# Optimization experiments

Measured on AMD Instinct MI355X. Metric: run time of the kernel, lower is better.

## Reference

```python
import jax, jax.numpy as jnp
import numpy as np

N = 4096      # num utterances (graph nodes)
D = 512       # utt_embed_size * 2
W = 10        # att_window_size
S = 8         # num speakers
WIN = 2 * W + 1


def setup_inputs() -> dict:
    key = jax.random.key(0)
    ks = jax.random.split(key, 7)
    s = 0.05  # keep activations in a sane range through two layers
    return {
        "context_embeds": jax.random.normal(ks[0], (N, D), jnp.float32),
        "speakers": jax.random.randint(ks[1], (N,), 0, S),
        "w_gc1": jax.random.normal(ks[2], (4, D, D), jnp.float32) * s,
        "w_gc2": jax.random.normal(ks[3], (4, D, D), jnp.float32) * s,
        "w_att": jax.random.normal(ks[4], (D, D), jnp.float32) * s,
        "w_aggr1": jax.random.normal(ks[5], (D, D), jnp.float32) * s,
        "w_aggr2": jax.random.normal(ks[6], (D, D), jnp.float32) * s,
    }


def _relation_adjs(x, speakers, w_att):
    """Windowed edge attention + 4 relation-masked adjacency matrices."""
    n = x.shape[0]
    pad = jnp.zeros((W, D), x.dtype)
    padded = jnp.concatenate([pad, x, pad], axis=0)          # [n+2W, D]
    # banded gather: row j sees padded[j : j+2W+1]  == cols j-W .. j+W
    gidx = jnp.arange(n)[:, None] + jnp.arange(WIN)[None, :]
    fat = padded[gidx]
    raw = jnp.einsum('nwd,ed->nwe', fat, w_att)               # Linear: x @ W^T
    scores = jnp.einsum('nwe,ne->nw', raw, x)
    attn = jax.nn.softmax(scores, axis=1)                     # softmax over full window (pads included, as original)
    # scatter attention into a banded [n, n] mask
    cols = jnp.arange(n)[:, None] + jnp.arange(WIN)[None, :] - W
    valid = (cols >= 0) & (cols < n)
    rows = jnp.broadcast_to(jnp.arange(n)[:, None], cols.shape)
    attn_mask = jnp.zeros((n, n), x.dtype).at[
        rows, jnp.clip(cols, 0, n - 1)].add(jnp.where(valid, attn, 0.0))
    i = jnp.arange(n)[:, None]
    j = jnp.arange(n)[None, :]
    band = jnp.abs(j - i) <= W
    same_spk = speakers[:, None] == speakers[None, :]
    pred = ((j >= i) & band).astype(x.dtype) * attn_mask      # successors-in-time kept (triu) within window
    suc = ((j < i) & band).astype(x.dtype) * attn_mask        # strict past within window
    same = (same_spk & band).astype(x.dtype) * attn_mask
    diff = ((~same_spk) & band).astype(x.dtype) * attn_mask
    return jnp.stack([pred, suc, same, diff])                 # [4, n, n]


def _gcn_layer(h, adjs, w_gc, w_aggr):
    # sum_r  A_r @ (h @ W_r)  + h @ W_aggr, then relu
    hw = jnp.einsum('md,rde->rme', h, w_gc)                   # [4, n, D]
    agg = jnp.einsum('rnm,rme->ne', adjs, hw)                 # [n, D]
    return jax.nn.relu(agg + h @ w_aggr)


def reference(context_embeds, speakers, w_gc1, w_gc2, w_att, w_aggr1, w_aggr2):
    adjs = _relation_adjs(context_embeds, speakers, w_att)
    h1 = _gcn_layer(context_embeds, adjs, w_gc1, w_aggr1)
    h2 = _gcn_layer(h1, adjs, w_gc2, w_aggr2)
    return h2
```

## Files before the change

### kernel.cpp

```cpp
#include <hip/hip_runtime.h>


#define NN 4096

typedef __bf16 bf16x8 __attribute__((ext_vector_type(8)));
typedef float f32x4 __attribute__((ext_vector_type(4)));
typedef unsigned short u16;
typedef unsigned int u32;

__device__ __forceinline__ u16 f2bf(float f) {
  unsigned u = __float_as_uint(f);
  unsigned r = u + 0x7FFFu + ((u >> 16) & 1u);
  return (u16)(r >> 16);
}
__device__ __forceinline__ float bf2f(u16 h) {
  return __uint_as_float(((unsigned)h) << 16);
}
__device__ __forceinline__ float blo(u32 v) { return __uint_as_float(v << 16); }
__device__ __forceinline__ float bhi(u32 v) { return __uint_as_float(v & 0xffff0000u); }
__device__ __forceinline__ u32 packbf(float a, float b) {
  return (u32)f2bf(a) | ((u32)f2bf(b) << 16);
}

__device__ __forceinline__ void gload_lds16(const u16* g, u16* l) {
  __builtin_amdgcn_global_load_lds(
      (const __attribute__((address_space(1))) void*)g,
      (__attribute__((address_space(3))) void*)l, 16, 0, 0);
}

__global__ void prep_all(const float* __restrict__ x, const float* __restrict__ w_att,
                         const float* __restrict__ w_gc1, const float* __restrict__ w_aggr1,
                         const float* __restrict__ w_gc2, const float* __restrict__ w_aggr2,
                         u16* __restrict__ Aatt, u16* __restrict__ Batt,
                         u16* __restrict__ Wt1, u16* __restrict__ Wt2,
                         float* __restrict__ xp, u32* __restrict__ xWg,
                         u32* __restrict__ h1Wg) {
  const int b = blockIdx.x, tid = threadIdx.x;
  if (b < 8192) {
    int idx = b * 256 + tid;
    int r = idx >> 9, c = idx & 511;
    float v = x[idx];
    u16 hi = f2bf(v), lo = f2bf(v - bf2f(hi));
    u16* row = Aatt + (size_t)r * 1536;
    row[c] = hi; row[512 + c] = lo; row[1024 + c] = hi;
    xp[(size_t)(r + 16) * 512 + c] = v;
  } else if (b < 9216) {
    int idx = (b - 8192) * 256 + tid;
    int j = idx >> 9, e = idx & 511;
    float v = w_att[(size_t)e * 512 + j];
    u16 hi = f2bf(v), lo = f2bf(v - bf2f(hi));
    u16* row = Batt + (size_t)j * 1536;
    row[e] = hi; row[512 + e] = hi; row[1024 + e] = lo;
  } else if (b < 17408) {
    int lay = (b >= 13312);
    int idx = (b - (lay ? 13312 : 9216)) * 256 + tid;
    const float* g = lay ? w_gc2 : w_gc1;
    const float* wa = lay ? w_aggr2 : w_aggr1;
    u16* Wt = lay ? Wt2 : Wt1;
    int j = idx >> 9, k = idx & 511;
    int p = j >> 9, jj = j & 511;
    size_t o = (size_t)k * 512 + jj;
    float v;
    if (p == 0)      v = g[o] - g[262144 + o];
    else if (p == 1) v = g[524288 + o] - g[786432 + o];
    else if (p == 2) v = g[262144 + o] + g[786432 + o];
    else             v = wa[o];
    Wt[(size_t)j * 512 + k] = f2bf(v);
  } else if (b < 17472) {
    int idx = (b - 17408) * 256 + tid;
    int g = idx >> 9, c = idx & 511;
    int row = (g < 16) ? g : 4112 + (g - 16);
    xp[(size_t)row * 512 + c] = 0.f;
  } else if (b < 17600) {
    int idx = (b - 17472) * 256 + tid;
    int g = idx >> 10, c = idx & 1023;
    int row = (g < 16) ? g : 4112 + (g - 16);
    xWg[(size_t)row * 1024 + c] = 0;
  } else {
    int idx = (b - 17600) * 256 + tid;
    int g = idx >> 10, c = idx & 1023;
    int row = (g < 16) ? g : 4112 + (g - 16);
    h1Wg[(size_t)row * 1024 + c] = 0;
  }
}

__device__ __forceinline__ void xcd_swz(int gx, int& bx, int& by) {
  int lid = by * gx + bx;
  int cpx = (gx * (int)gridDim.y) >> 3;
  int nl = (lid & 7) * cpx + (lid >> 3);
  by = nl / gx;
  bx = nl - by * gx;
}

__device__ __forceinline__ void gemm_core(const u16* __restrict__ A, const u16* __restrict__ Bt,
                                          int K, int lda, int ldb, size_t bm, size_t bn,
                                          u16 (&As)[2][8192], u16 (&Bs)[2][8192],
                                          f32x4 (&acc)[4][4]) {
  const int tid = threadIdx.x;
  const int lane = tid & 63;
  const int wave = tid >> 6;
  const int wr = wave >> 1, wc = wave & 1;
  const int arow = wr * 64 + (lane & 15);
  const int bcol = wc * 64 + (lane & 15);
  const int nt = K >> 6;

  auto STAGE = [&](int t, int bi) {
    const int k0 = t << 6;
#pragma unroll
    for (int c4 = 0; c4 < 4; ++c4) {
      const int o = (c4 * 256 + tid) * 16;
      const int r = o >> 7;
      const int sc = (((o >> 4) & 7) ^ (r & 7)) << 3;
      gload_lds16(A + (bm + r) * lda + k0 + sc, &As[bi][o >> 1]);
      gload_lds16(Bt + (bn + r) * ldb + k0 + sc, &Bs[bi][o >> 1]);
    }
  };

  STAGE(0, 0);
  for (int t = 0; t < nt; ++t) {
    const int cur = t & 1;
    if (t + 1 < nt) {
      STAGE(t + 1, cur ^ 1);
      asm volatile("s_waitcnt vmcnt(8)" ::: "memory");
    } else {
      asm volatile("s_waitcnt vmcnt(0)" ::: "memory");
    }
    __builtin_amdgcn_s_barrier();
    asm volatile("" ::: "memory");
    bf16x8 af[4][2], bfr[4][2];
#pragma unroll
    for (int i = 0; i < 4; ++i)
#pragma unroll
      for (int ks = 0; ks < 2; ++ks) {
        const int ar = arow + i * 16;
        const int ac = ((ks * 4 + (lane >> 4)) ^ (ar & 7)) << 4;
        af[i][ks] = *(const bf16x8*)((const char*)&As[cur][0] + ar * 128 + ac);
        const int br = bcol + i * 16;
        const int bc = ((ks * 4 + (lane >> 4)) ^ (br & 7)) << 4;
        bfr[i][ks] = *(const bf16x8*)((const char*)&Bs[cur][0] + br * 128 + bc);
      }
#pragma unroll
    for (int ks = 0; ks < 2; ++ks)
#pragma unroll
      for (int i = 0; i < 4; ++i)
#pragma unroll
        for (int j = 0; j < 4; ++j)
          acc[i][j] = __builtin_amdgcn_mfma_f32_16x16x32_bf16(af[i][ks], bfr[j][ks],
                                                              acc[i][j], 0, 0, 0);
    asm volatile("s_waitcnt lgkmcnt(0)" ::: "memory");
    __builtin_amdgcn_sched_barrier(0);
    __builtin_amdgcn_s_barrier();
  }
}

__global__ __launch_bounds__(256, 2) void fat_gemm(const u16* __restrict__ Aatt,
                                                   const u16* __restrict__ Wt1,
                                                   const u16* __restrict__ Batt,
                                                   u16* __restrict__ xW, float* __restrict__ y) {
  __shared__ u16 As[2][8192];
  __shared__ u16 Bs[2][8192];
  f32x4 acc[4][4] = {};
  const int tid = threadIdx.x;
  const int lane = tid & 63;
  const int wave = tid >> 6;
  const int wr = wave >> 1, wc = wave & 1;
  int bx = blockIdx.x, by = blockIdx.y;
  xcd_swz(20, bx, by);
  const size_t bm = (size_t)by * 128;
  const bool yp = bx < 4;
  const size_t bn = yp ? (size_t)bx * 128 : (size_t)(bx - 4) * 128;

  if (yp)
    gemm_core(Aatt, Batt, 1536, 1536, 1536, bm, bn, As, Bs, acc);
  else
    gemm_core(Aatt, Wt1, 512, 1536, 512, bm, bn, As, Bs, acc);

  const size_t crow = bm + wr * 64 + ((lane >> 4) * 4);
  const size_t ccol = bn + wc * 64 + (lane & 15);
#pragma unroll
  for (int i = 0; i < 4; ++i)
#pragma unroll
    for (int j = 0; j < 4; ++j)
#pragma unroll
      for (int b = 0; b < 4; ++b) {
        size_t r = crow + i * 16 + b, c = ccol + j * 16;
        if (yp)
          y[r * 512 + c] = acc[i][j][b];
        else
          xW[r * 2048 + c] = f2bf(acc[i][j][b]);
      }
}

__global__ __launch_bounds__(256, 2) void gemm_l2(const u16* __restrict__ h1,
                                                  const u16* __restrict__ Wt2,
                                                  u16* __restrict__ h1W) {
  __shared__ u16 As[2][8192];
  __shared__ u16 Bs[2][8192];
  f32x4 acc[4][4] = {};
  const int tid = threadIdx.x;
  const int lane = tid & 63;
  const int wave = tid >> 6;
  const int wr = wave >> 1, wc = wave & 1;
  int bx = blockIdx.x, by = blockIdx.y;
  xcd_swz(16, bx, by);
  const size_t bm = (size_t)by * 128;
  const size_t bn = (size_t)bx * 128;
  gemm_core(h1, Wt2, 512, 512, 512, bm, bn, As, Bs, acc);
  const size_t crow = bm + wr * 64 + ((lane >> 4) * 4);
  const size_t ccol = bn + wc * 64 + (lane & 15);
#pragma unroll
  for (int i = 0; i < 4; ++i)
#pragma unroll
    for (int j = 0; j < 4; ++j)
#pragma unroll
      for (int b = 0; b < 4; ++b) {
        size_t r = crow + i * 16 + b, c = ccol + j * 16;
        h1W[r * 2048 + c] = f2bf(acc[i][j][b]);
      }
}

__device__ __forceinline__ int xcd_row(int b) { return (b & 7) * 512 + (b >> 3); }

__global__ void gather1(const float* __restrict__ xp, const float* __restrict__ y,
                        const u16* __restrict__ xW, const int* __restrict__ spk,
                        float* __restrict__ attn, u16* __restrict__ h1) {
  const int n = xcd_row(blockIdx.x);
  const int tid = threadIdx.x;
  __shared__ float ys[512];
  __shared__ float sc[21];
  __shared__ float av[21], apv[21], asv[21];
  __shared__ int sps[21];
  const int mysp = spk[n];
  ys[tid] = y[(size_t)n * 512 + tid];
  ys[tid + 256] = y[(size_t)n * 512 + tid + 256];
  if (tid < 21) {
    int m = n + tid - 10;
    sps[tid] = (0 <= m && m < NN) ? spk[m] : -9;
  }
  __syncthreads();
  const int wave = tid >> 6, lane = tid & 63;
  for (int w = wave; w < 21; w += 4) {
    const float* xm = xp + (size_t)(n + 6 + w) * 512;
    float p = 0.f;
#pragma unroll
    for (int i = 0; i < 8; ++i) p += xm[lane + i * 64] * ys[lane + i * 64];
#pragma unroll
    for (int off = 32; off; off >>= 1) p += __shfl_xor(p, off, 64);
    if (lane == 0) sc[w] = p;
  }
  __syncthreads();
  if (tid < 64) {
    float v = (tid < 21) ? sc[tid] : -1e30f;
    float mx = v;
#pragma unroll
    for (int off = 32; off; off >>= 1) mx = fmaxf(mx, __shfl_xor(mx, off, 64));
    float e = (tid < 21) ? __expf(v - mx) : 0.f;
    float sum = e;
#pragma unroll
    for (int off = 32; off; off >>= 1) sum += __shfl_xor(sum, off, 64);
    if (tid < 21) {
      int m = n + tid - 10;
      float a = (0 <= m && m < NN) ? (e / sum) : 0.f;
      av[tid] = a;
      apv[tid] = (tid >= 10) ? a : 0.f;
      asv[tid] = (sps[tid] == mysp) ? a : 0.f;
      attn[(size_t)n * 24 + tid] = a;
    }
  }
  __syncthreads();
  const u32* xW32 = (const u32*)xW;
  u32 hv = xW32[(size_t)n * 1024 + 768 + tid];
  float a0 = blo(hv), a1 = bhi(hv);
#pragma unroll
  for (int w = 0; w < 10; ++w) {
    const u32* row = xW32 + (ptrdiff_t)(n - 10 + w) * 1024 + tid;
    u32 vs = row[256], va = row[512];
    float s2 = asv[w], a = av[w];
    a0 += s2 * blo(vs) + a * blo(va);
    a1 += s2 * bhi(vs) + a * bhi(va);
  }
#pragma unroll
  for (int w = 10; w < 21; ++w) {
    const u32* row = xW32 + (ptrdiff_t)(n - 10 + w) * 1024 + tid;
    u32 vp = row[0], vs = row[256], va = row[512];
    float ap = apv[w], s2 = asv[w], a = av[w];
    a0 += ap * blo(vp) + s2 * blo(vs) + a * blo(va);
    a1 += ap * bhi(vp) + s2 * bhi(vs) + a * bhi(va);
  }
  ((u32*)(h1 + (size_t)n * 512))[tid] = packbf(fmaxf(a0, 0.f), fmaxf(a1, 0.f));
}

__global__ void gather2(const u16* __restrict__ h1W, const float* __restrict__ attn,
                        const int* __restrict__ spk, float* __restrict__ out) {
  const int n = xcd_row(blockIdx.x);
  const int tid = threadIdx.x;
  __shared__ float av[21], apv[21], asv[21];
  if (tid < 21) {
    int m = n + tid - 10;
    float a = attn[(size_t)n * 24 + tid];
    int sp = (0 <= m && m < NN) ? spk[m] : -9;
    av[tid] = a;
    apv[tid] = (tid >= 10) ? a : 0.f;
    asv[tid] = (sp == spk[n]) ? a : 0.f;
  }
  __syncthreads();
  const u32* hW32 = (const u32*)h1W;
  u32 hv = hW32[(size_t)n * 1024 + 768 + tid];
  float a0 = blo(hv), a1 = bhi(hv);
#pragma unroll
  for (int w = 0; w < 10; ++w) {
    const u32* row = hW32 + (ptrdiff_t)(n - 10 + w) * 1024 + tid;
    u32 vs = row[256], va = row[512];
    float s2 = asv[w], a = av[w];
    a0 += s2 * blo(vs) + a * blo(va);
    a1 += s2 * bhi(vs) + a * bhi(va);
  }
#pragma unroll
  for (int w = 10; w < 21; ++w) {
    const u32* row = hW32 + (ptrdiff_t)(n - 10 + w) * 1024 + tid;
    u32 vp = row[0], vs = row[256], va = row[512];
    float ap = apv[w], s2 = asv[w], a = av[w];
    a0 += ap * blo(vp) + s2 * blo(vs) + a * blo(va);
    a1 += ap * bhi(vp) + s2 * bhi(vs) + a * bhi(va);
  }
  float* o = out + (size_t)n * 512 + tid * 2;
  o[0] = fmaxf(a0, 0.f);
  o[1] = fmaxf(a1, 0.f);
}

extern "C" void kernel_launch(void* const* d_in, const int* in_sizes, int n_in,
                              void* d_out, int out_size, void* d_ws, size_t ws_size,
                              hipStream_t stream) {
  const float* x = (const float*)d_in[0];
  const int* spk = (const int*)d_in[1];
  const float* w_gc1 = (const float*)d_in[2];
  const float* w_gc2 = (const float*)d_in[3];
  const float* w_att = (const float*)d_in[4];
  const float* w_aggr1 = (const float*)d_in[5];
  const float* w_aggr2 = (const float*)d_in[6];

  char* p = (char*)d_ws;
  u16* Aatt = (u16*)p;  p += (size_t)NN * 1536 * 2;
  u16* Batt = (u16*)p;  p += (size_t)512 * 1536 * 2;
  u16* Wt1 = (u16*)p;   p += (size_t)2048 * 512 * 2;
  u16* Wt2 = (u16*)p;   p += (size_t)2048 * 512 * 2;
  float* xp = (float*)p; p += (size_t)4128 * 512 * 4;
  float* y = (float*)p; p += (size_t)NN * 512 * 4;
  float* attn = (float*)p; p += (size_t)NN * 24 * 4;
  u16* xWg = (u16*)p;   p += (size_t)4128 * 2048 * 2;
  u16* h1 = (u16*)p;    p += (size_t)NN * 512 * 2;
  u16* h1Wg = (u16*)p;  p += (size_t)4128 * 2048 * 2;

  u16* xW = xWg + (size_t)16 * 2048;
  u16* h1W = h1Wg + (size_t)16 * 2048;

  prep_all<<<17728, 256, 0, stream>>>(x, w_att, w_gc1, w_aggr1, w_gc2, w_aggr2,
                                      Aatt, Batt, Wt1, Wt2, xp, (u32*)xWg, (u32*)h1Wg);

  fat_gemm<<<dim3(20, 32), 256, 0, stream>>>(Aatt, Wt1, Batt, xW, y);

  gather1<<<NN, 256, 0, stream>>>(xp, y, xW, spk, attn, h1);

  gemm_l2<<<dim3(16, 32), 256, 0, stream>>>(h1, Wt2, h1W);

  gather2<<<NN, 256, 0, stream>>>(h1W, attn, spk, (float*)d_out);
}
```

Measured before the change: 99.68 us.

## Split score softmax from band aggregation and tile aggregation over 8 rows

```diff
diff --git a/kernel.cpp b/kernel.cpp
--- a/kernel.cpp
+++ b/kernel.cpp
@@ -31,10 +31,11 @@
 __global__ void prep_all(const float* __restrict__ x, const float* __restrict__ w_att,
                          const float* __restrict__ w_gc1, const float* __restrict__ w_aggr1,
                          const float* __restrict__ w_gc2, const float* __restrict__ w_aggr2,
+                         const int* __restrict__ spk,
                          u16* __restrict__ Aatt, u16* __restrict__ Batt,
                          u16* __restrict__ Wt1, u16* __restrict__ Wt2,
                          float* __restrict__ xp, u32* __restrict__ xWg,
-                         u32* __restrict__ h1Wg) {
+                         u32* __restrict__ h1Wg, int* __restrict__ spkp) {
   const int b = blockIdx.x, tid = threadIdx.x;
   if (b < 8192) {
     int idx = b * 256 + tid;
@@ -76,11 +77,15 @@
     int g = idx >> 10, c = idx & 1023;
     int row = (g < 16) ? g : 4112 + (g - 16);
     xWg[(size_t)row * 1024 + c] = 0;
-  } else {
+  } else if (b < 17728) {
     int idx = (b - 17600) * 256 + tid;
     int g = idx >> 10, c = idx & 1023;
     int row = (g < 16) ? g : 4112 + (g - 16);
     h1Wg[(size_t)row * 1024 + c] = 0;
+  } else {
+    int idx = (b - 17728) * 256 + tid;
+    if (idx < 4128)
+      spkp[idx] = (idx >= 16 && idx < 4112) ? spk[idx - 16] : -9;
   }
 }
 
@@ -221,22 +226,14 @@
 
 __device__ __forceinline__ int xcd_row(int b) { return (b & 7) * 512 + (b >> 3); }
 
-__global__ void gather1(const float* __restrict__ xp, const float* __restrict__ y,
-                        const u16* __restrict__ xW, const int* __restrict__ spk,
-                        float* __restrict__ attn, u16* __restrict__ h1) {
+__global__ void scores_k(const float* __restrict__ xp, const float* __restrict__ y,
+                         float* __restrict__ attn) {
   const int n = xcd_row(blockIdx.x);
   const int tid = threadIdx.x;
   __shared__ float ys[512];
   __shared__ float sc[21];
-  __shared__ float av[21], apv[21], asv[21];
-  __shared__ int sps[21];
-  const int mysp = spk[n];
   ys[tid] = y[(size_t)n * 512 + tid];
   ys[tid + 256] = y[(size_t)n * 512 + tid + 256];
-  if (tid < 21) {
-    int m = n + tid - 10;
-    sps[tid] = (0 <= m && m < NN) ? spk[m] : -9;
-  }
   __syncthreads();
   const int wave = tid >> 6, lane = tid & 63;
   for (int w = wave; w < 21; w += 4) {
@@ -260,72 +257,70 @@
     for (int off = 32; off; off >>= 1) sum += __shfl_xor(sum, off, 64);
     if (tid < 21) {
       int m = n + tid - 10;
-      float a = (0 <= m && m < NN) ? (e / sum) : 0.f;
-      av[tid] = a;
-      apv[tid] = (tid >= 10) ? a : 0.f;
-      asv[tid] = (sps[tid] == mysp) ? a : 0.f;
-      attn[(size_t)n * 24 + tid] = a;
-    }
-  }
-  __syncthreads();
-  const u32* xW32 = (const u32*)xW;
-  u32 hv = xW32[(size_t)n * 1024 + 768 + tid];
-  float a0 = blo(hv), a1 = bhi(hv);
-#pragma unroll
-  for (int w = 0; w < 10; ++w) {
-    const u32* row = xW32 + (ptrdiff_t)(n - 10 + w) * 1024 + tid;
-    u32 vs = row[256], va = row[512];
-    float s2 = asv[w], a = av[w];
-    a0 += s2 * blo(vs) + a * blo(va);
-    a1 += s2 * bhi(vs) + a * bhi(va);
-  }
-#pragma unroll
-  for (int w = 10; w < 21; ++w) {
-    const u32* row = xW32 + (ptrdiff_t)(n - 10 + w) * 1024 + tid;
-    u32 vp = row[0], vs = row[256], va = row[512];
-    float ap = apv[w], s2 = asv[w], a = av[w];
-    a0 += ap * blo(vp) + s2 * blo(vs) + a * blo(va);
-    a1 += ap * bhi(vp) + s2 * bhi(vs) + a * bhi(va);
-  }
-  ((u32*)(h1 + (size_t)n * 512))[tid] = packbf(fmaxf(a0, 0.f), fmaxf(a1, 0.f));
-}
-
-__global__ void gather2(const u16* __restrict__ h1W, const float* __restrict__ attn,
-                        const int* __restrict__ spk, float* __restrict__ out) {
-  const int n = xcd_row(blockIdx.x);
-  const int tid = threadIdx.x;
-  __shared__ float av[21], apv[21], asv[21];
-  if (tid < 21) {
-    int m = n + tid - 10;
-    float a = attn[(size_t)n * 24 + tid];
-    int sp = (0 <= m && m < NN) ? spk[m] : -9;
-    av[tid] = a;
-    apv[tid] = (tid >= 10) ? a : 0.f;
-    asv[tid] = (sp == spk[n]) ? a : 0.f;
-  }
-  __syncthreads();
-  const u32* hW32 = (const u32*)h1W;
-  u32 hv = hW32[(size_t)n * 1024 + 768 + tid];
-  float a0 = blo(hv), a1 = bhi(hv);
-#pragma unroll
-  for (int w = 0; w < 10; ++w) {
-    const u32* row = hW32 + (ptrdiff_t)(n - 10 + w) * 1024 + tid;
-    u32 vs = row[256], va = row[512];
-    float s2 = asv[w], a = av[w];
-    a0 += s2 * blo(vs) + a * blo(va);
-    a1 += s2 * bhi(vs) + a * bhi(va);
-  }
-#pragma unroll
-  for (int w = 10; w < 21; ++w) {
-    const u32* row = hW32 + (ptrdiff_t)(n - 10 + w) * 1024 + tid;
-    u32 vp = row[0], vs = row[256], va = row[512];
-    float ap = apv[w], s2 = asv[w], a = av[w];
-    a0 += ap * blo(vp) + s2 * blo(vs) + a * blo(va);
-    a1 += ap * bhi(vp) + s2 * bhi(vs) + a * bhi(va);
-  }
-  float* o = out + (size_t)n * 512 + tid * 2;
-  o[0] = fmaxf(a0, 0.f);
-  o[1] = fmaxf(a1, 0.f);
+      attn[(size_t)n * 24 + tid] = (0 <= m && m < NN) ? (e / sum) : 0.f;
+    }
+  }
+}
+
+template <int OUT_BF16>
+__global__ __launch_bounds__(256) void bandagg(const u32* __restrict__ P32,
+                                               const float* __restrict__ attn,
+                                               const int* __restrict__ spkp,
+                                               void* __restrict__ out) {
+  const int b = blockIdx.x;
+  const int n0 = (((b & 7) << 6) + (b >> 3)) << 3;
+  const int tid = threadIdx.x;
+  const int* spk16 = spkp + 16;
+
+  int msp[8];
+#pragma unroll
+  for (int r = 0; r < 8; ++r) msp[r] = spk16[n0 + r];
+
+  float accL[8], accH[8];
+#pragma unroll
+  for (int r = 0; r < 8; ++r) {
+    u32 sv = P32[(size_t)(n0 + r) * 1024 + 768 + tid];
+    accL[r] = blo(sv);
+    accH[r] = bhi(sv);
+  }
+
+#pragma unroll
+  for (int j = 0; j < 28; ++j) {
+    const ptrdiff_t mrow = (ptrdiff_t)(n0 - 10 + j) * 1024;
+    u32 vp = P32[mrow + tid];
+    u32 vs = P32[mrow + 256 + tid];
+    u32 va = P32[mrow + 512 + tid];
+    float pl = blo(vp), ph = bhi(vp);
+    float sl = blo(vs), sh = bhi(vs);
+    float al = blo(va), ah = bhi(va);
+    const int mspk = spk16[n0 - 10 + j];
+#pragma unroll
+    for (int r = 0; r < 8; ++r) {
+      const int w = j - r;
+      if (w < 0 || w > 20) continue;
+      float a = attn[(size_t)(n0 + r) * 24 + w];
+      float as = (mspk == msp[r]) ? a : 0.f;
+      accL[r] += a * al;
+      accH[r] += a * ah;
+      accL[r] += as * sl;
+      accH[r] += as * sh;
+      if (w >= 10) {
+        accL[r] += a * pl;
+        accH[r] += a * ph;
+      }
+    }
+  }
+
+#pragma unroll
+  for (int r = 0; r < 8; ++r) {
+    float lo = fmaxf(accL[r], 0.f), hi = fmaxf(accH[r], 0.f);
+    if (OUT_BF16) {
+      ((u32*)out)[(size_t)(n0 + r) * 256 + tid] = packbf(lo, hi);
+    } else {
+      float2 v = {lo, hi};
+      ((float2*)out)[(size_t)(n0 + r) * 256 + tid] = v;
+    }
+  }
 }
 
 extern "C" void kernel_launch(void* const* d_in, const int* in_sizes, int n_in,
@@ -350,18 +345,22 @@
   u16* xWg = (u16*)p;   p += (size_t)4128 * 2048 * 2;
   u16* h1 = (u16*)p;    p += (size_t)NN * 512 * 2;
   u16* h1Wg = (u16*)p;  p += (size_t)4128 * 2048 * 2;
+  int* spkp = (int*)p;  p += (size_t)4128 * 4;
 
   u16* xW = xWg + (size_t)16 * 2048;
   u16* h1W = h1Wg + (size_t)16 * 2048;
 
-  prep_all<<<17728, 256, 0, stream>>>(x, w_att, w_gc1, w_aggr1, w_gc2, w_aggr2,
-                                      Aatt, Batt, Wt1, Wt2, xp, (u32*)xWg, (u32*)h1Wg);
+  prep_all<<<17745, 256, 0, stream>>>(x, w_att, w_gc1, w_aggr1, w_gc2, w_aggr2, spk,
+                                      Aatt, Batt, Wt1, Wt2, xp, (u32*)xWg, (u32*)h1Wg,
+                                      spkp);
 
   fat_gemm<<<dim3(20, 32), 256, 0, stream>>>(Aatt, Wt1, Batt, xW, y);
 
-  gather1<<<NN, 256, 0, stream>>>(xp, y, xW, spk, attn, h1);
+  scores_k<<<NN, 256, 0, stream>>>(xp, y, attn);
+
+  bandagg<1><<<512, 256, 0, stream>>>((const u32*)xW, attn, spkp, h1);
 
   gemm_l2<<<dim3(16, 32), 256, 0, stream>>>(h1, Wt2, h1W);
 
-  gather2<<<NN, 256, 0, stream>>>(h1W, attn, spk, (float*)d_out);
-}
+  bandagg<0><<<512, 256, 0, stream>>>((const u32*)h1W, attn, spkp, d_out);
+}
```

Result: slower. 104.2 us (+4.6%).

## Align XCD row ownership across kernels and pad speaker array

Applied to the files above, without the earlier changes.

```diff
diff --git a/kernel.cpp b/kernel.cpp
--- a/kernel.cpp
+++ b/kernel.cpp
@@ -31,15 +31,17 @@
 __global__ void prep_all(const float* __restrict__ x, const float* __restrict__ w_att,
                          const float* __restrict__ w_gc1, const float* __restrict__ w_aggr1,
                          const float* __restrict__ w_gc2, const float* __restrict__ w_aggr2,
+                         const int* __restrict__ spk,
                          u16* __restrict__ Aatt, u16* __restrict__ Batt,
                          u16* __restrict__ Wt1, u16* __restrict__ Wt2,
                          float* __restrict__ xp, u32* __restrict__ xWg,
-                         u32* __restrict__ h1Wg) {
+                         u32* __restrict__ h1Wg, int* __restrict__ spkp) {
   const int b = blockIdx.x, tid = threadIdx.x;
   if (b < 8192) {
-    int idx = b * 256 + tid;
-    int r = idx >> 9, c = idx & 511;
-    float v = x[idx];
+    int s = b >> 3;
+    int r = 512 * (b & 7) + (s >> 1);
+    int c = ((s & 1) << 8) + tid;
+    float v = x[(size_t)r * 512 + c];
     u16 hi = f2bf(v), lo = f2bf(v - bf2f(hi));
     u16* row = Aatt + (size_t)r * 1536;
     row[c] = hi; row[512 + c] = lo; row[1024 + c] = hi;
@@ -76,20 +78,25 @@
     int g = idx >> 10, c = idx & 1023;
     int row = (g < 16) ? g : 4112 + (g - 16);
     xWg[(size_t)row * 1024 + c] = 0;
-  } else {
+  } else if (b < 17728) {
     int idx = (b - 17600) * 256 + tid;
     int g = idx >> 10, c = idx & 1023;
     int row = (g < 16) ? g : 4112 + (g - 16);
     h1Wg[(size_t)row * 1024 + c] = 0;
-  }
-}
-
-__device__ __forceinline__ void xcd_swz(int gx, int& bx, int& by) {
+  } else {
+    int idx = (b - 17728) * 256 + tid;
+    if (idx < 4128)
+      spkp[idx] = (idx >= 16 && idx < 4112) ? spk[idx - 16] : -9;
+  }
+}
+
+__device__ __forceinline__ void xcd_align(int gx, int& bx, int& by) {
   int lid = by * gx + bx;
-  int cpx = (gx * (int)gridDim.y) >> 3;
-  int nl = (lid & 7) * cpx + (lid >> 3);
-  by = nl / gx;
-  bx = nl - by * gx;
+  int xcd = lid & 7;
+  int s = lid >> 3;
+  int q = s / gx;
+  bx = s - q * gx;
+  by = xcd * 4 + q;
 }
 
 __device__ __forceinline__ void gemm_core(const u16* __restrict__ A, const u16* __restrict__ Bt,
@@ -165,7 +172,7 @@
   const int wave = tid >> 6;
   const int wr = wave >> 1, wc = wave & 1;
   int bx = blockIdx.x, by = blockIdx.y;
-  xcd_swz(20, bx, by);
+  xcd_align(20, bx, by);
   const size_t bm = (size_t)by * 128;
   const bool yp = bx < 4;
   const size_t bn = yp ? (size_t)bx * 128 : (size_t)(bx - 4) * 128;
@@ -202,7 +209,7 @@
   const int wave = tid >> 6;
   const int wr = wave >> 1, wc = wave & 1;
   int bx = blockIdx.x, by = blockIdx.y;
-  xcd_swz(16, bx, by);
+  xcd_align(16, bx, by);
   const size_t bm = (size_t)by * 128;
   const size_t bn = (size_t)bx * 128;
   gemm_core(h1, Wt2, 512, 512, 512, bm, bn, As, Bs, acc);
@@ -222,7 +229,7 @@
 __device__ __forceinline__ int xcd_row(int b) { return (b & 7) * 512 + (b >> 3); }
 
 __global__ void gather1(const float* __restrict__ xp, const float* __restrict__ y,
-                        const u16* __restrict__ xW, const int* __restrict__ spk,
+                        const u16* __restrict__ xW, const int* __restrict__ spkp,
                         float* __restrict__ attn, u16* __restrict__ h1) {
   const int n = xcd_row(blockIdx.x);
   const int tid = threadIdx.x;
@@ -230,13 +237,10 @@
   __shared__ float sc[21];
   __shared__ float av[21], apv[21], asv[21];
   __shared__ int sps[21];
-  const int mysp = spk[n];
+  const int mysp = spkp[16 + n];
   ys[tid] = y[(size_t)n * 512 + tid];
   ys[tid + 256] = y[(size_t)n * 512 + tid + 256];
-  if (tid < 21) {
-    int m = n + tid - 10;
-    sps[tid] = (0 <= m && m < NN) ? spk[m] : -9;
-  }
+  if (tid < 21) sps[tid] = spkp[16 + n - 10 + tid];
   __syncthreads();
   const int wave = tid >> 6, lane = tid & 63;
   for (int w = wave; w < 21; w += 4) {
@@ -291,17 +295,16 @@
 }
 
 __global__ void gather2(const u16* __restrict__ h1W, const float* __restrict__ attn,
-                        const int* __restrict__ spk, float* __restrict__ out) {
+                        const int* __restrict__ spkp, float* __restrict__ out) {
   const int n = xcd_row(blockIdx.x);
   const int tid = threadIdx.x;
   __shared__ float av[21], apv[21], asv[21];
   if (tid < 21) {
-    int m = n + tid - 10;
     float a = attn[(size_t)n * 24 + tid];
-    int sp = (0 <= m && m < NN) ? spk[m] : -9;
+    int sp = spkp[16 + n - 10 + tid];
     av[tid] = a;
     apv[tid] = (tid >= 10) ? a : 0.f;
-    asv[tid] = (sp == spk[n]) ? a : 0.f;
+    asv[tid] = (sp == spkp[16 + n]) ? a : 0.f;
   }
   __syncthreads();
   const u32* hW32 = (const u32*)h1W;
@@ -350,18 +353,20 @@
   u16* xWg = (u16*)p;   p += (size_t)4128 * 2048 * 2;
   u16* h1 = (u16*)p;    p += (size_t)NN * 512 * 2;
   u16* h1Wg = (u16*)p;  p += (size_t)4128 * 2048 * 2;
+  int* spkp = (int*)p;  p += (size_t)4128 * 4;
 
   u16* xW = xWg + (size_t)16 * 2048;
   u16* h1W = h1Wg + (size_t)16 * 2048;
 
-  prep_all<<<17728, 256, 0, stream>>>(x, w_att, w_gc1, w_aggr1, w_gc2, w_aggr2,
-                                      Aatt, Batt, Wt1, Wt2, xp, (u32*)xWg, (u32*)h1Wg);
+  prep_all<<<17745, 256, 0, stream>>>(x, w_att, w_gc1, w_aggr1, w_gc2, w_aggr2, spk,
+                                      Aatt, Batt, Wt1, Wt2, xp, (u32*)xWg, (u32*)h1Wg,
+                                      spkp);
 
   fat_gemm<<<dim3(20, 32), 256, 0, stream>>>(Aatt, Wt1, Batt, xW, y);
 
-  gather1<<<NN, 256, 0, stream>>>(xp, y, xW, spk, attn, h1);
+  gather1<<<NN, 256, 0, stream>>>(xp, y, xW, spkp, attn, h1);
 
   gemm_l2<<<dim3(16, 32), 256, 0, stream>>>(h1, Wt2, h1W);
 
-  gather2<<<NN, 256, 0, stream>>>(h1W, attn, spk, (float*)d_out);
-}
+  gather2<<<NN, 256, 0, stream>>>(h1W, attn, spkp, (float*)d_out);
+}
```

Measured after the change: 99.19 us. Within noise of the previous version (-0.5%).
